# Performance work log

Measured on AMD Instinct MI355X. Metric: run time of the kernel, lower is better.

## Reference

```python
import jax, jax.numpy as jnp
import numpy as np
from jax import lax

EMBED_DIM = 384
NUM_GROUPS = 128
GROUP_SIZE = 64
LN_EPS = 1e-5


def setup_inputs() -> dict:
    key = jax.random.key(0)
    k_pts, k1, k2, k3, k4 = jax.random.split(key, 5)
    B, N = 32, 16384
    points = jax.random.normal(k_pts, (B, N, 3), dtype=jnp.float32)
    # local_mlp: Linear(3,128) -> GELU -> Linear(128, embed_dim)
    w1 = jax.random.normal(k1, (3, 128), dtype=jnp.float32) * (1.0 / np.sqrt(3))
    b1 = jax.random.normal(k2, (128,), dtype=jnp.float32) * 0.01
    w2 = jax.random.normal(k3, (128, EMBED_DIM), dtype=jnp.float32) * (1.0 / np.sqrt(128))
    b2 = jax.random.normal(k4, (EMBED_DIM,), dtype=jnp.float32) * 0.01
    ln_scale = jnp.ones((EMBED_DIM,), dtype=jnp.float32)
    ln_bias = jnp.zeros((EMBED_DIM,), dtype=jnp.float32)
    return {"points": points, "w1": w1, "b1": b1, "w2": w2, "b2": b2,
            "ln_scale": ln_scale, "ln_bias": ln_bias}


def _farthest_point_sample(points, num_samples):
    # points: [B, N, 3]. Deterministic start at index 0 (torch uses randint).
    B, N, _ = points.shape

    def step(carry, _):
        distance, farthest = carry  # [B, N], [B]
        centroid = jnp.take_along_axis(points, farthest[:, None, None], axis=1)  # [B,1,3]
        d = jnp.sum((points - centroid) ** 2, axis=-1)  # [B, N]
        distance = jnp.minimum(distance, d)
        nxt = jnp.argmax(distance, axis=-1).astype(jnp.int32)
        return (distance, nxt), farthest

    init = (jnp.full((B, N), jnp.inf, dtype=points.dtype),
            jnp.zeros((B,), dtype=jnp.int32))
    _, idx = lax.scan(step, init, None, length=num_samples)  # [S, B]
    return idx.T  # [B, S]


def reference(points, w1, b1, w2, b2, ln_scale, ln_bias):
    B, N, _ = points.shape
    centroid_idx = _farthest_point_sample(points, NUM_GROUPS)  # [B, G]
    centroids = jnp.take_along_axis(
        points, centroid_idx[:, :, None].astype(jnp.int32), axis=1)  # [B, G, 3]

    # squared distances (same ordering as torch.cdist for topk); matmul form
    # avoids materializing a [B, G, N, 3] diff tensor.
    c2 = jnp.sum(centroids ** 2, axis=-1)  # [B, G]
    p2 = jnp.sum(points ** 2, axis=-1)     # [B, N]
    dist2 = c2[:, :, None] + p2[:, None, :] - 2.0 * jnp.einsum(
        'bgc,bnc->bgn', centroids, points)  # [B, G, N]

    # k smallest -> top_k of negated distances
    _, neighbor_idx = lax.top_k(-dist2, GROUP_SIZE)  # [B, G, K]

    batch_ix = jnp.arange(B)[:, None, None]
    grouped = points[batch_ix, neighbor_idx]  # [B, G, K, 3]
    local_coords = grouped - centroids[:, :, None, :]  # [B, G, K, 3]

    h = jax.nn.gelu(local_coords @ w1 + b1, approximate=False)  # [B,G,K,128]
    feats = h @ w2 + b2  # [B, G, K, D]
    tokens = jnp.mean(feats, axis=2)  # [B, G, D]

    mu = jnp.mean(tokens, axis=-1, keepdims=True)
    var = jnp.mean((tokens - mu) ** 2, axis=-1, keepdims=True)
    tokens_ln = (tokens - mu) * lax.rsqrt(var + LN_EPS) * ln_scale + ln_bias
    return centroids, tokens_ln
```

## Files before the change

kernel.cpp:

```cpp
#include <hip/hip_runtime.h>
#include <math.h>

#define BB 32
#define NN 16384
#define GG 128
#define KK 64
#define HH 128
#define DD 384
#define LN_EPS 1e-5f
#define NBUCK 2048
#define CANDCAP 1024

__device__ __forceinline__ float sq3(float x, float y, float z) {
    return __fadd_rn(__fadd_rn(__fmul_rn(x, x), __fmul_rn(y, y)), __fmul_rn(z, z));
}

__device__ __forceinline__ unsigned distkey(float px, float py, float pz, float4 c4) {
    float p2 = sq3(px, py, pz);
    float dot = __fadd_rn(__fadd_rn(__fmul_rn(c4.x, px), __fmul_rn(c4.y, py)),
                          __fmul_rn(c4.z, pz));
    float d = __fsub_rn(__fadd_rn(c4.w, p2), __fmul_rn(2.0f, dot));
    unsigned u = __float_as_uint(d);
    return u ^ ((u & 0x80000000u) ? 0xFFFFFFFFu : 0x80000000u);
}

__global__ void prep_kernel(const float* __restrict__ w2, float* __restrict__ w2t) {
    int i = blockIdx.x * 256 + threadIdx.x;
    if (i < HH * DD) {
        int f = i >> 7;
        int k = i & 127;
        w2t[i] = w2[k * DD + f];
    }
}

__global__ __launch_bounds__(512, 2) void fps_kernel(const float* __restrict__ pts,
                                                     float* __restrict__ cent_out,
                                                     float4* __restrict__ cent_pad) {
    const int b = blockIdx.x;
    const int tid = threadIdx.x;
    const float* p = pts + (size_t)b * NN * 3;
    const float4* p4 = (const float4*)p;

    float x[32], y[32], z[32], dist[32];
#pragma unroll
    for (int j = 0; j < 8; j++) {
        int q = j * 512 + tid;
        float4 A = p4[3 * q], B = p4[3 * q + 1], C = p4[3 * q + 2];
        x[j * 4 + 0] = A.x; y[j * 4 + 0] = A.y; z[j * 4 + 0] = A.z;
        x[j * 4 + 1] = A.w; y[j * 4 + 1] = B.x; z[j * 4 + 1] = B.y;
        x[j * 4 + 2] = B.z; y[j * 4 + 2] = B.w; z[j * 4 + 2] = C.x;
        x[j * 4 + 3] = C.y; y[j * 4 + 3] = C.z; z[j * 4 + 3] = C.w;
    }
#pragma unroll
    for (int r = 0; r < 32; r++) {
        asm volatile("" : "+v"(x[r]), "+v"(y[r]), "+v"(z[r]));
        dist[r] = INFINITY;
    }

    __shared__ unsigned long long slot[GG];
    for (int i = tid; i < GG; i += 512) slot[i] = 0ull;
    __syncthreads();

    float cx = p[0], cy = p[1], cz = p[2];

    for (int it = 0; it < GG; it++) {
        if (tid == 0) {
            float* co = cent_out + ((size_t)b * GG + it) * 3;
            co[0] = cx; co[1] = cy; co[2] = cz;
            cent_pad[b * GG + it] = make_float4(cx, cy, cz, sq3(cx, cy, cz));
        }
        if (it == GG - 1) break;

        float bv0 = -INFINITY, bv1 = -INFINITY, bv2 = -INFINITY, bv3 = -INFINITY;
        int bi0 = 0, bi1 = 0, bi2 = 0, bi3 = 0;
#pragma unroll
        for (int j = 0; j < 8; j++) {
            int nb = 4 * (j * 512 + tid);
#pragma unroll
            for (int t = 0; t < 4; t++) {
                int r = j * 4 + t;
                float dx = __fsub_rn(x[r], cx);
                float dy = __fsub_rn(y[r], cy);
                float dz = __fsub_rn(z[r], cz);
                float d = sq3(dx, dy, dz);
                float dj = fminf(dist[r], d);
                dist[r] = dj;
                int n = nb + t;
                switch (t) {
                    case 0: if (dj > bv0) { bv0 = dj; bi0 = n; } break;
                    case 1: if (dj > bv1) { bv1 = dj; bi1 = n; } break;
                    case 2: if (dj > bv2) { bv2 = dj; bi2 = n; } break;
                    case 3: if (dj > bv3) { bv3 = dj; bi3 = n; } break;
                }
            }
        }
        float fv = bv0; int fi = bi0;
        if (bv1 > fv || (bv1 == fv && bi1 < fi)) { fv = bv1; fi = bi1; }
        if (bv2 > fv || (bv2 == fv && bi2 < fi)) { fv = bv2; fi = bi2; }
        if (bv3 > fv || (bv3 == fv && bi3 < fi)) { fv = bv3; fi = bi3; }
#pragma unroll
        for (int off = 32; off >= 1; off >>= 1) {
            float ov = __shfl_down(fv, off);
            int oi = __shfl_down(fi, off);
            if (ov > fv || (ov == fv && oi < fi)) { fv = ov; fi = oi; }
        }
        if ((tid & 63) == 0) {
            unsigned long long packed =
                ((unsigned long long)__float_as_uint(fv) << 32) |
                (unsigned)(0xFFFFFFFFu - (unsigned)fi);
            atomicMax(&slot[it], packed);
        }
        __syncthreads();
        unsigned long long w = slot[it];
        int idx = (int)(0xFFFFFFFFu - (unsigned)w);
        const float* wp = p + (size_t)idx * 3;
        cx = wp[0]; cy = wp[1]; cz = wp[2];
    }
}

__global__ __launch_bounds__(256, 4) void group_kernel(
    const float* __restrict__ pts, const float4* __restrict__ cent_pad,
    const float* __restrict__ w1, const float* __restrict__ b1,
    const float* __restrict__ w2t, const float* __restrict__ b2,
    const float* __restrict__ lns, const float* __restrict__ lnb,
    float* __restrict__ tok_out) {
    __shared__ __align__(16) unsigned keyLds[NN];
    __shared__ __align__(16) union {
        unsigned hist[NBUCK];
        unsigned long long cand[CANDCAP];
    } sh;
    __shared__ int selIdx[KK];
    __shared__ float4 localPt[KK];
    __shared__ float w1s[3 * HH];
    __shared__ float b1s[HH];
    __shared__ __align__(16) float hbar[HH];
    __shared__ float partial[256];
    __shared__ float red2[8];
    __shared__ float toks[DD];
    __shared__ int waveSum[4];
    __shared__ unsigned long long wmin[4];
    __shared__ unsigned TA_S;
    __shared__ int cntS;
    __shared__ unsigned long long lastS;
    __shared__ float muS, rstdS;

    const int tid = threadIdx.x;
    int bid = blockIdx.x;
    int xcd = bid & 7, sub = bid >> 3;
    int b = xcd * 4 + (sub >> 7);
    int g = sub & 127;

    const float* p = pts + (size_t)b * NN * 3;
    const float4* p4 = (const float4*)p;
    float4 c4 = cent_pad[b * GG + g];

    for (int i = tid; i < 3 * HH; i += 256) w1s[i] = w1[i];
    if (tid < HH) b1s[tid] = b1[tid];
    for (int i = tid; i < NBUCK; i += 256) sh.hist[i] = 0;
    if (tid == 0) cntS = 0;
    __syncthreads();

    for (int i = 0; i < 16; i++) {
        int t4 = i * 256 + tid;
        float4 A = p4[3 * t4], B = p4[3 * t4 + 1], C = p4[3 * t4 + 2];
        unsigned k0 = distkey(A.x, A.y, A.z, c4);
        unsigned k1 = distkey(A.w, B.x, B.y, c4);
        unsigned k2 = distkey(B.z, B.w, C.x, c4);
        unsigned k3 = distkey(C.y, C.z, C.w, c4);
        ((uint4*)keyLds)[t4] = make_uint4(k0, k1, k2, k3);
        atomicAdd(&sh.hist[k0 >> 21], 1u);
        atomicAdd(&sh.hist[k1 >> 21], 1u);
        atomicAdd(&sh.hist[k2 >> 21], 1u);
        atomicAdd(&sh.hist[k3 >> 21], 1u);
    }
    __syncthreads();

    {
        uint4 h0 = ((const uint4*)sh.hist)[tid * 2];
        uint4 h1 = ((const uint4*)sh.hist)[tid * 2 + 1];
        int loc[8] = {(int)h0.x, (int)h0.y, (int)h0.z, (int)h0.w,
                      (int)h1.x, (int)h1.y, (int)h1.z, (int)h1.w};
        int s = 0;
#pragma unroll
        for (int j = 0; j < 8; j++) s += loc[j];
        int lane = tid & 63, wid = tid >> 6;
        int v = s;
#pragma unroll
        for (int off = 1; off < 64; off <<= 1) {
            int o = __shfl_up(v, off);
            if (lane >= off) v += o;
        }
        if (lane == 63) waveSum[wid] = v;
        __syncthreads();
        int base = 0;
        for (int w = 0; w < wid; w++) base += waveSum[w];
        int c = base + v - s;
#pragma unroll
        for (int j = 0; j < 8; j++) {
            if (c < KK && c + loc[j] >= KK) TA_S = (unsigned)(tid * 8 + j);
            c += loc[j];
        }
        __syncthreads();
    }
    unsigned TA = TA_S;

    for (int i = 0; i < 16; i++) {
        int t4 = i * 256 + tid;
        uint4 kv = ((const uint4*)keyLds)[t4];
        unsigned kk[4] = {kv.x, kv.y, kv.z, kv.w};
#pragma unroll
        for (int q = 0; q < 4; q++) {
            if ((kk[q] >> 21) <= TA) {
                int pos = atomicAdd(&cntS, 1);
                if (pos < CANDCAP)
                    sh.cand[pos] =
                        ((unsigned long long)kk[q] << 32) | (unsigned)(4 * t4 + q);
            }
        }
    }
    __syncthreads();
    int cnt = cntS;

    if (cnt <= CANDCAP) {
        for (int c0 = tid; c0 < cnt; c0 += 256) {
            unsigned long long pr = sh.cand[c0];
            int rank = 0;
            for (int j = 0; j < cnt; j++) rank += (sh.cand[j] < pr);
            if (rank < KK) selIdx[rank] = (int)(unsigned)pr;
        }
        __syncthreads();
    } else {
        if (tid == 0) lastS = 0ull;
        __syncthreads();
        for (int r = 0; r < KK; r++) {
            unsigned long long last = lastS;
            unsigned long long best = 0xFFFFFFFFFFFFFFFFull;
            for (int i = 0; i < 64; i++) {
                int n = i * 256 + tid;
                unsigned long long pr =
                    ((unsigned long long)keyLds[n] << 32) | (unsigned)n;
                if ((r == 0 || pr > last) && pr < best) best = pr;
            }
            unsigned blo = (unsigned)best, bhi = (unsigned)(best >> 32);
#pragma unroll
            for (int off = 32; off >= 1; off >>= 1) {
                unsigned olo = __shfl_down(blo, off);
                unsigned ohi = __shfl_down(bhi, off);
                unsigned long long ob = ((unsigned long long)ohi << 32) | olo;
                unsigned long long cur = ((unsigned long long)bhi << 32) | blo;
                if (ob < cur) { blo = olo; bhi = ohi; }
            }
            int lane = tid & 63, wid = tid >> 6;
            if (lane == 0) wmin[wid] = ((unsigned long long)bhi << 32) | blo;
            __syncthreads();
            if (tid == 0) {
                unsigned long long m = wmin[0];
                for (int w = 1; w < 4; w++) if (wmin[w] < m) m = wmin[w];
                selIdx[r] = (int)(unsigned)m;
                lastS = m;
            }
            __syncthreads();
        }
    }

    if (tid < KK) {
        int n = selIdx[tid];
        float px = p[n * 3], py = p[n * 3 + 1], pz = p[n * 3 + 2];
        localPt[tid] = make_float4(px - c4.x, py - c4.y, pz - c4.z, 0.f);
    }
    __syncthreads();
    {
        int f = tid & 127, half = tid >> 7;
        float wa = w1s[f], wb = w1s[HH + f], wc = w1s[2 * HH + f], bb = b1s[f];
        float s = 0.f;
        for (int k = half * 32; k < half * 32 + 32; k++) {
            float4 lp = localPt[k];
            float a = lp.x * wa + lp.y * wb + lp.z * wc + bb;
            float hh = 0.5f * a * (1.0f + erff(a * 0.70710678118654752440f));
            s += hh;
        }
        partial[tid] = s;
    }
    __syncthreads();
    if (tid < HH) hbar[tid] = (partial[tid] + partial[tid + HH]) * (1.0f / 64.0f);
    __syncthreads();
    for (int f2 = tid; f2 < DD; f2 += 256) {
        const float4* wrow = (const float4*)(w2t + f2 * HH);
        const float4* hb = (const float4*)hbar;
        float acc = b2[f2];
#pragma unroll 8
        for (int q = 0; q < 32; q++) {
            float4 w4 = wrow[q];
            float4 h4 = hb[q];
            acc += h4.x * w4.x + h4.y * w4.y + h4.z * w4.z + h4.w * w4.w;
        }
        toks[f2] = acc;
    }
    __syncthreads();
    {
        float s1 = 0.f, s2 = 0.f;
        for (int f2 = tid; f2 < DD; f2 += 256) {
            float v = toks[f2];
            s1 += v;
            s2 += v * v;
        }
#pragma unroll
        for (int off = 32; off >= 1; off >>= 1) {
            s1 += __shfl_down(s1, off);
            s2 += __shfl_down(s2, off);
        }
        int lane = tid & 63, wid = tid >> 6;
        if (lane == 0) { partial[wid] = s1; red2[wid] = s2; }
        __syncthreads();
        if (tid == 0) {
            float t1 = partial[0] + partial[1] + partial[2] + partial[3];
            float t2 = red2[0] + red2[1] + red2[2] + red2[3];
            float mu = t1 / (float)DD;
            float var = t2 / (float)DD - mu * mu;
            muS = mu;
            rstdS = rsqrtf(var + LN_EPS);
        }
        __syncthreads();
    }
    float mu = muS, rstd = rstdS;
    float* outp = tok_out + ((size_t)b * GG + g) * DD;
    for (int f2 = tid; f2 < DD; f2 += 256) {
        outp[f2] = (toks[f2] - mu) * rstd * lns[f2] + lnb[f2];
    }
}

extern "C" void kernel_launch(void* const* d_in, const int* in_sizes, int n_in,
                              void* d_out, int out_size, void* d_ws, size_t ws_size,
                              hipStream_t stream) {
    const float* pts = (const float*)d_in[0];
    const float* w1 = (const float*)d_in[1];
    const float* b1 = (const float*)d_in[2];
    const float* w2 = (const float*)d_in[3];
    const float* b2 = (const float*)d_in[4];
    const float* lns = (const float*)d_in[5];
    const float* lnb = (const float*)d_in[6];
    float* out = (float*)d_out;

    float4* cent_pad = (float4*)d_ws;
    float* w2t = (float*)((char*)d_ws + BB * GG * sizeof(float4));

    prep_kernel<<<192, 256, 0, stream>>>(w2, w2t);
    fps_kernel<<<BB, 512, 0, stream>>>(pts, out, cent_pad);
    group_kernel<<<BB * GG, 256, 0, stream>>>(pts, cent_pad, w1, b1, w2t, b2, lns, lnb,
                                              out + BB * GG * 3);
}
```

Measured before the change: 567.6 us.

## Replace histogram kNN selection with sampled threshold and wave bitonic sort

The group kernel no longer stores all 16384 keys and builds a 2048-bucket histogram in LDS. It sorts a 256-point sample to estimate a threshold (8th or 64th smallest sample key), keeps candidates under that threshold, and picks the top 64 with wave-level bitonic sort and merge. This cuts LDS use from about 80KB to about 25KB, which should raise occupancy and remove histogram atomics. The cost is recomputing distances when the first threshold yields too few candidates, and a slower fallback path. FPS also moves to 1024 threads with 16 points per thread held in named registers.

Result: slower. 634.9 us (+11.9%).

```diff
diff --git a/kernel.cpp b/kernel.cpp
--- a/kernel.cpp
+++ b/kernel.cpp
@@ -8,8 +8,7 @@
 #define HH 128
 #define DD 384
 #define LN_EPS 1e-5f
-#define NBUCK 2048
-#define CANDCAP 1024
+#define CANDCAP 2560
 
 __device__ __forceinline__ float sq3(float x, float y, float z) {
     return __fadd_rn(__fadd_rn(__fmul_rn(x, x), __fmul_rn(y, y)), __fmul_rn(z, z));
@@ -24,6 +23,38 @@
     return u ^ ((u & 0x80000000u) ? 0xFFFFFFFFu : 0x80000000u);
 }
 
+__device__ __forceinline__ void sort64(unsigned& k, unsigned& i) {
+    const int lane = threadIdx.x & 63;
+#pragma unroll
+    for (int m = 2; m <= 64; m <<= 1) {
+#pragma unroll
+        for (int j = m >> 1; j > 0; j >>= 1) {
+            unsigned ok = __shfl_xor(k, j, 64);
+            unsigned oi = __shfl_xor(i, j, 64);
+            bool lt = (ok < k) || (ok == k && oi < i);
+            bool low = ((lane & j) == 0);
+            bool asc = ((lane & m) == 0);
+            if ((low == asc) ? lt : !lt) { k = ok; i = oi; }
+        }
+    }
+}
+
+__device__ __forceinline__ void merge64(unsigned& k, unsigned& i, unsigned kB, unsigned iB) {
+    const int lane = threadIdx.x & 63;
+    unsigned rk = __shfl(kB, 63 - lane, 64);
+    unsigned ri = __shfl(iB, 63 - lane, 64);
+    bool lt = (rk < k) || (rk == k && ri < i);
+    if (lt) { k = rk; i = ri; }
+#pragma unroll
+    for (int j = 32; j > 0; j >>= 1) {
+        unsigned ok = __shfl_xor(k, j, 64);
+        unsigned oi = __shfl_xor(i, j, 64);
+        bool l2 = (ok < k) || (ok == k && oi < i);
+        bool low = ((lane & j) == 0);
+        if (low ? l2 : !l2) { k = ok; i = oi; }
+    }
+}
+
 __global__ void prep_kernel(const float* __restrict__ w2, float* __restrict__ w2t) {
     int i = blockIdx.x * 256 + threadIdx.x;
     if (i < HH * DD) {
@@ -33,32 +64,47 @@
     }
 }
 
-__global__ __launch_bounds__(512, 2) void fps_kernel(const float* __restrict__ pts,
-                                                     float* __restrict__ cent_out,
-                                                     float4* __restrict__ cent_pad) {
+#define FPS_DECL(r) float x##r, y##r, z##r, d##r;
+#define FPS_LOAD(j, r0, r1, r2, r3)                                        \
+    {                                                                      \
+        int q = (j)*1024 + tid;                                            \
+        float4 A = p4[3 * q], B = p4[3 * q + 1], C = p4[3 * q + 2];        \
+        x##r0 = A.x; y##r0 = A.y; z##r0 = A.z;                             \
+        x##r1 = A.w; y##r1 = B.x; z##r1 = B.y;                             \
+        x##r2 = B.z; y##r2 = B.w; z##r2 = C.x;                             \
+        x##r3 = C.y; y##r3 = C.z; z##r3 = C.w;                             \
+        d##r0 = INFINITY; d##r1 = INFINITY; d##r2 = INFINITY; d##r3 = INFINITY; \
+    }
+#define FPS_UPD(r, base, c)                                                \
+    {                                                                      \
+        float dx = __fsub_rn(x##r, cx);                                    \
+        float dy = __fsub_rn(y##r, cy);                                    \
+        float dz = __fsub_rn(z##r, cz);                                    \
+        float dd = sq3(dx, dy, dz);                                        \
+        float dj = fminf(d##r, dd);                                        \
+        d##r = dj;                                                         \
+        if (dj > bv##c) { bv##c = dj; bi##c = (base) + 4 * tid; }          \
+    }
+
+__global__ __launch_bounds__(1024, 4) void fps_kernel(const float* __restrict__ pts,
+                                                      float* __restrict__ cent_out,
+                                                      float4* __restrict__ cent_pad) {
     const int b = blockIdx.x;
     const int tid = threadIdx.x;
     const float* p = pts + (size_t)b * NN * 3;
     const float4* p4 = (const float4*)p;
 
-    float x[32], y[32], z[32], dist[32];
-#pragma unroll
-    for (int j = 0; j < 8; j++) {
-        int q = j * 512 + tid;
-        float4 A = p4[3 * q], B = p4[3 * q + 1], C = p4[3 * q + 2];
-        x[j * 4 + 0] = A.x; y[j * 4 + 0] = A.y; z[j * 4 + 0] = A.z;
-        x[j * 4 + 1] = A.w; y[j * 4 + 1] = B.x; z[j * 4 + 1] = B.y;
-        x[j * 4 + 2] = B.z; y[j * 4 + 2] = B.w; z[j * 4 + 2] = C.x;
-        x[j * 4 + 3] = C.y; y[j * 4 + 3] = C.z; z[j * 4 + 3] = C.w;
-    }
-#pragma unroll
-    for (int r = 0; r < 32; r++) {
-        asm volatile("" : "+v"(x[r]), "+v"(y[r]), "+v"(z[r]));
-        dist[r] = INFINITY;
-    }
+    FPS_DECL(0) FPS_DECL(1) FPS_DECL(2) FPS_DECL(3)
+    FPS_DECL(4) FPS_DECL(5) FPS_DECL(6) FPS_DECL(7)
+    FPS_DECL(8) FPS_DECL(9) FPS_DECL(10) FPS_DECL(11)
+    FPS_DECL(12) FPS_DECL(13) FPS_DECL(14) FPS_DECL(15)
+    FPS_LOAD(0, 0, 1, 2, 3)
+    FPS_LOAD(1, 4, 5, 6, 7)
+    FPS_LOAD(2, 8, 9, 10, 11)
+    FPS_LOAD(3, 12, 13, 14, 15)
 
     __shared__ unsigned long long slot[GG];
-    for (int i = tid; i < GG; i += 512) slot[i] = 0ull;
+    for (int i = tid; i < GG; i += 1024) slot[i] = 0ull;
     __syncthreads();
 
     float cx = p[0], cy = p[1], cz = p[2];
@@ -73,27 +119,11 @@
 
         float bv0 = -INFINITY, bv1 = -INFINITY, bv2 = -INFINITY, bv3 = -INFINITY;
         int bi0 = 0, bi1 = 0, bi2 = 0, bi3 = 0;
-#pragma unroll
-        for (int j = 0; j < 8; j++) {
-            int nb = 4 * (j * 512 + tid);
-#pragma unroll
-            for (int t = 0; t < 4; t++) {
-                int r = j * 4 + t;
-                float dx = __fsub_rn(x[r], cx);
-                float dy = __fsub_rn(y[r], cy);
-                float dz = __fsub_rn(z[r], cz);
-                float d = sq3(dx, dy, dz);
-                float dj = fminf(dist[r], d);
-                dist[r] = dj;
-                int n = nb + t;
-                switch (t) {
-                    case 0: if (dj > bv0) { bv0 = dj; bi0 = n; } break;
-                    case 1: if (dj > bv1) { bv1 = dj; bi1 = n; } break;
-                    case 2: if (dj > bv2) { bv2 = dj; bi2 = n; } break;
-                    case 3: if (dj > bv3) { bv3 = dj; bi3 = n; } break;
-                }
-            }
-        }
+        FPS_UPD(0, 0, 0)      FPS_UPD(1, 1, 1)      FPS_UPD(2, 2, 2)      FPS_UPD(3, 3, 3)
+        FPS_UPD(4, 4096, 0)   FPS_UPD(5, 4097, 1)   FPS_UPD(6, 4098, 2)   FPS_UPD(7, 4099, 3)
+        FPS_UPD(8, 8192, 0)   FPS_UPD(9, 8193, 1)   FPS_UPD(10, 8194, 2)  FPS_UPD(11, 8195, 3)
+        FPS_UPD(12, 12288, 0) FPS_UPD(13, 12289, 1) FPS_UPD(14, 12290, 2) FPS_UPD(15, 12291, 3)
+
         float fv = bv0; int fi = bi0;
         if (bv1 > fv || (bv1 == fv && bi1 < fi)) { fv = bv1; fi = bi1; }
         if (bv2 > fv || (bv2 == fv && bi2 < fi)) { fv = bv2; fi = bi2; }
@@ -124,11 +154,8 @@
     const float* __restrict__ w2t, const float* __restrict__ b2,
     const float* __restrict__ lns, const float* __restrict__ lnb,
     float* __restrict__ tok_out) {
-    __shared__ __align__(16) unsigned keyLds[NN];
-    __shared__ __align__(16) union {
-        unsigned hist[NBUCK];
-        unsigned long long cand[CANDCAP];
-    } sh;
+    __shared__ __align__(16) unsigned long long cand[CANDCAP];
+    __shared__ unsigned long long runLds[256];
     __shared__ int selIdx[KK];
     __shared__ float4 localPt[KK];
     __shared__ float w1s[3 * HH];
@@ -137,14 +164,14 @@
     __shared__ float partial[256];
     __shared__ float red2[8];
     __shared__ float toks[DD];
-    __shared__ int waveSum[4];
     __shared__ unsigned long long wmin[4];
-    __shared__ unsigned TA_S;
+    __shared__ unsigned T1S, T2S;
     __shared__ int cntS;
     __shared__ unsigned long long lastS;
     __shared__ float muS, rstdS;
 
     const int tid = threadIdx.x;
+    const int lane = tid & 63, wid = tid >> 6;
     int bid = blockIdx.x;
     int xcd = bid & 7, sub = bid >> 3;
     int b = xcd * 4 + (sub >> 7);
@@ -156,76 +183,91 @@
 
     for (int i = tid; i < 3 * HH; i += 256) w1s[i] = w1[i];
     if (tid < HH) b1s[tid] = b1[tid];
-    for (int i = tid; i < NBUCK; i += 256) sh.hist[i] = 0;
     if (tid == 0) cntS = 0;
-    __syncthreads();
-
-    for (int i = 0; i < 16; i++) {
-        int t4 = i * 256 + tid;
-        float4 A = p4[3 * t4], B = p4[3 * t4 + 1], C = p4[3 * t4 + 2];
-        unsigned k0 = distkey(A.x, A.y, A.z, c4);
-        unsigned k1 = distkey(A.w, B.x, B.y, c4);
-        unsigned k2 = distkey(B.z, B.w, C.x, c4);
-        unsigned k3 = distkey(C.y, C.z, C.w, c4);
-        ((uint4*)keyLds)[t4] = make_uint4(k0, k1, k2, k3);
-        atomicAdd(&sh.hist[k0 >> 21], 1u);
-        atomicAdd(&sh.hist[k1 >> 21], 1u);
-        atomicAdd(&sh.hist[k2 >> 21], 1u);
-        atomicAdd(&sh.hist[k3 >> 21], 1u);
-    }
-    __syncthreads();
 
     {
-        uint4 h0 = ((const uint4*)sh.hist)[tid * 2];
-        uint4 h1 = ((const uint4*)sh.hist)[tid * 2 + 1];
-        int loc[8] = {(int)h0.x, (int)h0.y, (int)h0.z, (int)h0.w,
-                      (int)h1.x, (int)h1.y, (int)h1.z, (int)h1.w};
-        int s = 0;
-#pragma unroll
-        for (int j = 0; j < 8; j++) s += loc[j];
-        int lane = tid & 63, wid = tid >> 6;
-        int v = s;
-#pragma unroll
-        for (int off = 1; off < 64; off <<= 1) {
-            int o = __shfl_up(v, off);
-            if (lane >= off) v += o;
-        }
-        if (lane == 63) waveSum[wid] = v;
-        __syncthreads();
-        int base = 0;
-        for (int w = 0; w < wid; w++) base += waveSum[w];
-        int c = base + v - s;
-#pragma unroll
-        for (int j = 0; j < 8; j++) {
-            if (c < KK && c + loc[j] >= KK) TA_S = (unsigned)(tid * 8 + j);
-            c += loc[j];
-        }
-        __syncthreads();
-    }
-    unsigned TA = TA_S;
-
-    for (int i = 0; i < 16; i++) {
-        int t4 = i * 256 + tid;
-        uint4 kv = ((const uint4*)keyLds)[t4];
-        unsigned kk[4] = {kv.x, kv.y, kv.z, kv.w};
-#pragma unroll
-        for (int q = 0; q < 4; q++) {
-            if ((kk[q] >> 21) <= TA) {
-                int pos = atomicAdd(&cntS, 1);
-                if (pos < CANDCAP)
-                    sh.cand[pos] =
-                        ((unsigned long long)kk[q] << 32) | (unsigned)(4 * t4 + q);
-            }
-        }
-    }
+        int sn = tid << 6;
+        unsigned sk = distkey(p[sn * 3], p[sn * 3 + 1], p[sn * 3 + 2], c4);
+        unsigned si = (unsigned)sn;
+        sort64(sk, si);
+        runLds[tid] = ((unsigned long long)sk << 32) | si;
+        __syncthreads();
+        if (wid == 0) {
+            unsigned ak = sk, ai = si;
+#pragma unroll
+            for (int w = 1; w < 4; w++) {
+                unsigned long long v = runLds[w * 64 + lane];
+                merge64(ak, ai, (unsigned)(v >> 32), (unsigned)v);
+            }
+            if (lane == 7) T1S = ak;
+            if (lane == 63) T2S = ak;
+        }
+        __syncthreads();
+    }
+
+#define COLLECT(TT)                                                            \
+    for (int i = 0; i < 16; i++) {                                             \
+        int t4 = i * 256 + tid;                                                \
+        float4 A = p4[3 * t4], Bv = p4[3 * t4 + 1], Cv = p4[3 * t4 + 2];       \
+        unsigned kks[4];                                                       \
+        kks[0] = distkey(A.x, A.y, A.z, c4);                                   \
+        kks[1] = distkey(A.w, Bv.x, Bv.y, c4);                                 \
+        kks[2] = distkey(Bv.z, Bv.w, Cv.x, c4);                                \
+        kks[3] = distkey(Cv.y, Cv.z, Cv.w, c4);                                \
+        _Pragma("unroll") for (int q = 0; q < 4; q++) {                        \
+            if (kks[q] <= (TT)) {                                              \
+                int pos = atomicAdd(&cntS, 1);                                 \
+                if (pos < CANDCAP)                                             \
+                    cand[pos] = ((unsigned long long)kks[q] << 32) |           \
+                                (unsigned)(4 * t4 + q);                        \
+            }                                                                  \
+        }                                                                      \
+    }
+
+    unsigned T1 = T1S;
+    COLLECT(T1)
     __syncthreads();
     int cnt = cntS;
 
-    if (cnt <= CANDCAP) {
+    if (cnt < KK) {
+        if (tid == 0) cntS = 0;
+        __syncthreads();
+        unsigned T2 = T2S;
+        COLLECT(T2)
+        __syncthreads();
+        cnt = cntS;
+    }
+
+    if (cnt >= KK && cnt <= 1024) {
+        unsigned ak, ai;
+#pragma unroll
+        for (int r = 0; r < 4; r++) {
+            int slot16 = (wid * 4 + r) * 64 + lane;
+            unsigned ck = 0xFFFFFFFFu, ci = 0xFFFFFFFFu;
+            if (slot16 < cnt) {
+                unsigned long long v = cand[slot16];
+                ck = (unsigned)(v >> 32); ci = (unsigned)v;
+            }
+            sort64(ck, ci);
+            if (r == 0) { ak = ck; ai = ci; }
+            else merge64(ak, ai, ck, ci);
+        }
+        runLds[tid] = ((unsigned long long)ak << 32) | ai;
+        __syncthreads();
+        if (wid == 0) {
+#pragma unroll
+            for (int w = 1; w < 4; w++) {
+                unsigned long long v = runLds[w * 64 + lane];
+                merge64(ak, ai, (unsigned)(v >> 32), (unsigned)v);
+            }
+            selIdx[lane] = (int)ai;
+        }
+        __syncthreads();
+    } else if (cnt >= KK && cnt <= CANDCAP) {
         for (int c0 = tid; c0 < cnt; c0 += 256) {
-            unsigned long long pr = sh.cand[c0];
+            unsigned long long pr = cand[c0];
             int rank = 0;
-            for (int j = 0; j < cnt; j++) rank += (sh.cand[j] < pr);
+            for (int j = 0; j < cnt; j++) rank += (cand[j] < pr);
             if (rank < KK) selIdx[rank] = (int)(unsigned)pr;
         }
         __syncthreads();
@@ -235,11 +277,20 @@
         for (int r = 0; r < KK; r++) {
             unsigned long long last = lastS;
             unsigned long long best = 0xFFFFFFFFFFFFFFFFull;
-            for (int i = 0; i < 64; i++) {
-                int n = i * 256 + tid;
-                unsigned long long pr =
-                    ((unsigned long long)keyLds[n] << 32) | (unsigned)n;
-                if ((r == 0 || pr > last) && pr < best) best = pr;
+            for (int i = 0; i < 16; i++) {
+                int t4 = i * 256 + tid;
+                float4 A = p4[3 * t4], Bv = p4[3 * t4 + 1], Cv = p4[3 * t4 + 2];
+                unsigned kks[4];
+                kks[0] = distkey(A.x, A.y, A.z, c4);
+                kks[1] = distkey(A.w, Bv.x, Bv.y, c4);
+                kks[2] = distkey(Bv.z, Bv.w, Cv.x, c4);
+                kks[3] = distkey(Cv.y, Cv.z, Cv.w, c4);
+#pragma unroll
+                for (int q = 0; q < 4; q++) {
+                    unsigned long long pr =
+                        ((unsigned long long)kks[q] << 32) | (unsigned)(4 * t4 + q);
+                    if ((r == 0 || pr > last) && pr < best) best = pr;
+                }
             }
             unsigned blo = (unsigned)best, bhi = (unsigned)(best >> 32);
 #pragma unroll
@@ -250,7 +301,6 @@
                 unsigned long long cur = ((unsigned long long)bhi << 32) | blo;
                 if (ob < cur) { blo = olo; bhi = ohi; }
             }
-            int lane = tid & 63, wid = tid >> 6;
             if (lane == 0) wmin[wid] = ((unsigned long long)bhi << 32) | blo;
             __syncthreads();
             if (tid == 0) {
@@ -309,7 +359,6 @@
             s1 += __shfl_down(s1, off);
             s2 += __shfl_down(s2, off);
         }
-        int lane = tid & 63, wid = tid >> 6;
         if (lane == 0) { partial[wid] = s1; red2[wid] = s2; }
         __syncthreads();
         if (tid == 0) {
@@ -345,7 +394,7 @@
     float* w2t = (float*)((char*)d_ws + BB * GG * sizeof(float4));
 
     prep_kernel<<<192, 256, 0, stream>>>(w2, w2t);
-    fps_kernel<<<BB, 512, 0, stream>>>(pts, out, cent_pad);
+    fps_kernel<<<BB, 1024, 0, stream>>>(pts, out, cent_pad);
     group_kernel<<<BB * GG, 256, 0, stream>>>(pts, cent_pad, w1, b1, w2t, b2, lns, lnb,
                                               out + BB * GG * 3);
 }
```
